# Performance work log

Hardware: AMD Instinct MI355X
Metric: run time of the kernel (lower is better)

The kernel has to match this reference:

```python
import jax, jax.numpy as jnp
import numpy as np

HEADS = 12
WINDOW = 128

def setup_inputs() -> dict:
    key = jax.random.key(0)
    ks = jax.random.split(key, 5)
    B, N, C = 1, 4096, 768
    return {
        'x': jax.random.normal(ks[0], (B, N, C), dtype=jnp.float32),
        'qkv_w': jax.random.normal(ks[1], (3 * C, C), dtype=jnp.float32) * 0.02,
        'qkv_b': jax.random.normal(ks[2], (3 * C,), dtype=jnp.float32) * 0.02,
        'proj_w': jax.random.normal(ks[3], (C, C), dtype=jnp.float32) * 0.02,
        'proj_b': jax.random.normal(ks[4], (C,), dtype=jnp.float32) * 0.02,
    }

def reference(x, qkv_w, qkv_b, proj_w, proj_b):
    B, N, C = x.shape
    H = HEADS
    hd = C // H
    # qkv projection (torch Linear: y = x @ W^T + b)
    qkv = x @ qkv_w.T + qkv_b                      # [B, N, 3C]
    qkv = qkv.reshape(B, N, 3, H, hd).transpose(2, 0, 3, 1, 4)  # [3, B, H, N, hd]
    q, k, v = qkv[0], qkv[1], qkv[2]               # each [B, H, N, hd]
    # local (banded) mask: |i - j| <= window_size
    idxs = jnp.arange(N)
    local = jnp.abs(idxs[:, None] - idxs[None, :]) <= WINDOW  # [N, N] bool
    # dense scores then mask (faithful to original O(N^2) math)
    attn = jnp.einsum('bhnd,bhmd->bhnm', q, k) / jnp.sqrt(jnp.float32(hd))
    attn = jnp.where(local[None, None], attn, -jnp.inf)
    attn = jax.nn.softmax(attn, axis=-1)
    out = jnp.einsum('bhnm,bhmd->bhnd', attn, v)   # [B, H, N, hd]
    out = out.transpose(0, 2, 1, 3).reshape(B, N, C)
    return out @ proj_w.T + proj_b
```

## Files before the change

### kernel.cpp

```cpp
#include <hip/hip_runtime.h>
#include <hip/hip_fp16.h>
#include <cmath>

typedef _Float16 f16;
typedef __attribute__((ext_vector_type(8))) _Float16 f16x8;
typedef __attribute__((ext_vector_type(4))) _Float16 f16x4;
typedef __attribute__((ext_vector_type(4))) float f32x4;

#define EXP2F(x) __builtin_amdgcn_exp2f(x)

__global__ void pack3_f32_f16(
    const float* __restrict__ s0, f16* __restrict__ d0, int nc0, int kc0,
    const float* __restrict__ s1, f16* __restrict__ d1, int nc1, int kc1,
    const float* __restrict__ s2, f16* __restrict__ d2, int nc2, int kc2)
{
    int wid  = (blockIdx.x * blockDim.x + threadIdx.x) >> 6;
    int lane = threadIdx.x & 63;
    const float* s; f16* d; int cid, KC;
    if (wid < nc0)                  { s = s0; d = d0; cid = wid;             KC = kc0; }
    else if (wid < nc0 + nc1)       { s = s1; d = d1; cid = wid - nc0;       KC = kc1; }
    else if (wid < nc0 + nc1 + nc2) { s = s2; d = d2; cid = wid - nc0 - nc1; KC = kc2; }
    else return;
    int rc = cid / KC, kc = cid % KC;
    int K  = KC << 5;
    const float* src = s + (size_t)(rc * 16 + (lane & 15)) * K + kc * 32 + (lane >> 4) * 8;
    float4 v0 = *(const float4*)src;
    float4 v1 = *(const float4*)(src + 4);
    f16x8 o = { (f16)v0.x, (f16)v0.y, (f16)v0.z, (f16)v0.w,
                (f16)v1.x, (f16)v1.y, (f16)v1.z, (f16)v1.w };
    *(f16x8*)(d + (size_t)cid * 512 + lane * 8) = o;
}

__device__ __forceinline__ void store4(f16* p, const f32x4& v) {
    f16x4 o = { (f16)v[0], (f16)v[1], (f16)v[2], (f16)v[3] };
    *(f16x4*)p = o;
}
__device__ __forceinline__ void store4(float* p, const f32x4& v) {
    float4 o = { v[0], v[1], v[2], v[3] };
    *(float4*)p = o;
}

template <int WR, int WC, int MT, int NT, int MODE, typename OT>
__global__ __launch_bounds__(256) void gemm_f16_packed(
    const f16* __restrict__ Ap,
    const f16* __restrict__ Wp,
    const float* __restrict__ bias,
    OT* __restrict__ out,
    int M, int N, int K)
{
    constexpr int KK  = 2;
    constexpr int ACH = WR * MT * KK;
    constexpr int BCH = WC * NT * KK;
    constexpr int AR  = ACH / 4;
    constexpr int BR  = BCH / 4;
    __shared__ f16 Ash[2][ACH * 512];
    __shared__ f16 Bsh[2][BCH * 512];

    const int tid  = threadIdx.x;
    const int lane = tid & 63;
    const int w    = tid >> 6;
    const int wr   = w / WC;
    const int wc   = w % WC;
    const int lr   = lane & 15;
    const int lq   = lane >> 4;
    const int bm   = blockIdx.y * (WR * MT * 16);
    const int bn   = blockIdx.x * (WC * NT * 16);
    const int KC   = K >> 5;

    const f16* ga[AR];
    const f16* gb[BR];
#pragma unroll
    for (int r = 0; r < AR; ++r) {
        int s = w * AR + r, rl = s / KK, kk = s % KK;
        ga[r] = Ap + ((size_t)((bm >> 4) + rl) * KC + kk) * 512 + lane * 8;
    }
#pragma unroll
    for (int r = 0; r < BR; ++r) {
        int s = w * BR + r, rl = s / KK, kk = s % KK;
        gb[r] = Wp + ((size_t)((bn >> 4) + rl) * KC + kk) * 512 + lane * 8;
    }

    f32x4 acc[MT][NT] = {};
    f16x8 sa[AR], sb[BR];

#pragma unroll
    for (int r = 0; r < AR; ++r) sa[r] = *(const f16x8*)(ga[r]);
#pragma unroll
    for (int r = 0; r < BR; ++r) sb[r] = *(const f16x8*)(gb[r]);
#pragma unroll
    for (int r = 0; r < AR; ++r) *(f16x8*)&Ash[0][(w * AR + r) * 512 + lane * 8] = sa[r];
#pragma unroll
    for (int r = 0; r < BR; ++r) *(f16x8*)&Bsh[0][(w * BR + r) * 512 + lane * 8] = sb[r];
    __syncthreads();

    const int nk = K >> 6;
    for (int k = 0; k < nk; ++k) {
        const int cur = k & 1;
        if (k + 1 < nk) {
            const int ko = (k + 1) * KK * 512;
#pragma unroll
            for (int r = 0; r < AR; ++r) sa[r] = *(const f16x8*)(ga[r] + ko);
#pragma unroll
            for (int r = 0; r < BR; ++r) sb[r] = *(const f16x8*)(gb[r] + ko);
        }
        f16x8 af[MT][KK], bf[NT][KK];
#pragma unroll
        for (int mt = 0; mt < MT; ++mt)
#pragma unroll
            for (int kk = 0; kk < KK; ++kk)
                af[mt][kk] = *(const f16x8*)&Ash[cur][((wr * MT + mt) * KK + kk) * 512 + lane * 8];
#pragma unroll
        for (int nt = 0; nt < NT; ++nt)
#pragma unroll
            for (int kk = 0; kk < KK; ++kk)
                bf[nt][kk] = *(const f16x8*)&Bsh[cur][((wc * NT + nt) * KK + kk) * 512 + lane * 8];
#pragma unroll
        for (int kk = 0; kk < KK; ++kk)
#pragma unroll
            for (int mt = 0; mt < MT; ++mt)
#pragma unroll
                for (int nt = 0; nt < NT; ++nt)
                    acc[mt][nt] = __builtin_amdgcn_mfma_f32_16x16x32_f16(
                        bf[nt][kk], af[mt][kk], acc[mt][nt], 0, 0, 0);
        if (k + 1 < nk) {
#pragma unroll
            for (int r = 0; r < AR; ++r)
                *(f16x8*)&Ash[cur ^ 1][(w * AR + r) * 512 + lane * 8] = sa[r];
#pragma unroll
            for (int r = 0; r < BR; ++r)
                *(f16x8*)&Bsh[cur ^ 1][(w * BR + r) * 512 + lane * 8] = sb[r];
        }
        __syncthreads();
    }

#pragma unroll
    for (int mt = 0; mt < MT; ++mt) {
        int row = bm + (wr * MT + mt) * 16 + lr;
#pragma unroll
        for (int nt = 0; nt < NT; ++nt) {
            int col = bn + (wc * NT + nt) * 16 + lq * 4;
            float4 bv = *(const float4*)(bias + col);
            f32x4 ov = acc[mt][nt];
            ov[0] += bv.x; ov[1] += bv.y; ov[2] += bv.z; ov[3] += bv.w;
            if (MODE == 0) {
                store4(out + (size_t)row * N + col, ov);
            } else {
                int tau = (col >= 1536) ? 2 : (col >= 768 ? 1 : 0);
                int rm  = col - tau * 768;
                int hh  = rm >> 6;
                int d   = rm & 63;
                f16* base = (f16*)out + ((size_t)tau * 12 + hh) * ((size_t)M * 64);
                if (tau < 2) {
                    size_t off = (size_t)(row >> 4) * 1024 + (d >> 5) * 512
                               + (size_t)((row & 15) + ((d >> 3) & 3) * 16) * 8 + (d & 7);
                    store4(base + off, ov);
                } else {
#pragma unroll
                    for (int i = 0; i < 4; ++i) {
                        int dd = d + i;
                        size_t off = (size_t)(dd >> 4) * ((size_t)M * 16)
                                   + (size_t)(row >> 5) * 512
                                   + (size_t)((dd & 15) + ((row >> 3) & 3) * 16) * 8 + (row & 7);
                        base[off] = (f16)ov[i];
                    }
                }
            }
        }
    }
}

#define WINDOW_SZ 128

__global__ __launch_bounds__(256) void local_attn_mfma(
    const f16* __restrict__ qkvp,
    f16* __restrict__ outp,
    int N)
{
    const int C = 768;
    __shared__ f16 Ps[4096];

    const int tid  = threadIdx.x;
    const int lane = tid & 63;
    const int w    = tid >> 6;
    const int r15  = lane & 15;
    const int q4   = lane >> 4;
    const int ntiles = N >> 6;
    const int h  = blockIdx.x / ntiles;
    const int i0 = (blockIdx.x % ntiles) << 6;

    const size_t hstride = (size_t)N * 64;
    const f16* Qh = qkvp + (size_t)h * hstride;
    const f16* Kh = qkvp + (size_t)(12 + h) * hstride;
    const f16* Vh = qkvp + (size_t)(24 + h) * hstride;
    const int dcStride = N * 16;

    f16x8 qf[2];
    {
        const f16* qp = Qh + (size_t)((i0 >> 4) + w) * 1024 + lane * 8;
        qf[0] = *(const f16x8*)(qp);
        qf[1] = *(const f16x8*)(qp + 512);
        const f16 qs = (f16)0.18033688f;
#pragma unroll
        for (int j = 0; j < 8; ++j) { qf[0][j] *= qs; qf[1][j] *= qs; }
    }

    f32x4 o[4] = {};
    float m_l = -1.0e30f, l_l = 0.f;

    const int lo = (i0 >= 128) ? 0 : ((128 - i0) >> 6);
    int hi = (N + 64 - i0) >> 6; if (hi > 4) hi = 4;

    const int lssr = lane ^ ((lane >> 3) & 7);

    for (int ch = lo; ch <= hi; ++ch) {
        const int jbase = i0 - 128 + ch * 64;
        const bool need_mask = (ch == 0) || (ch == 4);

        f32x4 s[4] = {};
#pragma unroll
        for (int ks = 0; ks < 2; ++ks)
#pragma unroll
            for (int nt = 0; nt < 4; ++nt) {
                f16x8 kf = *(const f16x8*)(Kh + (size_t)((jbase >> 4) + nt) * 1024
                                              + ks * 512 + lane * 8);
                s[nt] = __builtin_amdgcn_mfma_f32_16x16x32_f16(kf, qf[ks], s[nt], 0, 0, 0);
            }

        if (need_mask) {
            int qg = i0 + w * 16 + r15;
#pragma unroll
            for (int nt = 0; nt < 4; ++nt)
#pragma unroll
                for (int r = 0; r < 4; ++r) {
                    int dist = qg - (jbase + nt * 16 + q4 * 4 + r);
                    if (dist < 0) dist = -dist;
                    if (dist > WINDOW_SZ) s[nt][r] = -3.0e38f;
                }
        }

        float rmax = -3.0e38f;
#pragma unroll
        for (int nt = 0; nt < 4; ++nt)
#pragma unroll
            for (int r = 0; r < 4; ++r) rmax = fmaxf(rmax, s[nt][r]);
        rmax = fmaxf(rmax, __shfl_xor(rmax, 16));
        rmax = fmaxf(rmax, __shfl_xor(rmax, 32));
        float mn = fmaxf(m_l, rmax);
        float al = EXP2F(m_l - mn);
        m_l = mn;
        float rs = 0.f;
#pragma unroll
        for (int nt = 0; nt < 4; ++nt)
#pragma unroll
            for (int r = 0; r < 4; ++r) {
                float pv = EXP2F(s[nt][r] - mn);
                s[nt][r] = pv;
                rs += pv;
            }
        rs += __shfl_xor(rs, 16);
        rs += __shfl_xor(rs, 32);
        l_l = l_l * al + rs;
#pragma unroll
        for (int nd = 0; nd < 4; ++nd)
#pragma unroll
            for (int r = 0; r < 4; ++r) o[nd][r] *= al;

#pragma unroll
        for (int nt = 0; nt < 4; ++nt)
#pragma unroll
            for (int r = 0; r < 4; ++r) {
                int c  = nt * 16 + q4 * 4 + r;
                int cs = c >> 5;
                int c5 = c & 31;
                int ls = (c5 >> 3) * 16 + r15;
                int lss = ls ^ ((ls >> 3) & 7);
                Ps[(w * 2 + cs) * 512 + lss * 8 + (c5 & 7)] = (f16)s[nt][r];
            }

#pragma unroll
        for (int cs = 0; cs < 2; ++cs) {
            f16x8 pf = *(const f16x8*)&Ps[(w * 2 + cs) * 512 + lssr * 8];
#pragma unroll
            for (int nd = 0; nd < 4; ++nd) {
                f16x8 vf = *(const f16x8*)(Vh + (size_t)nd * dcStride
                                              + (size_t)((jbase >> 5) + cs) * 512 + lane * 8);
                o[nd] = __builtin_amdgcn_mfma_f32_16x16x32_f16(vf, pf, o[nd], 0, 0, 0);
            }
        }
    }

    float inv = 1.0f / l_l;
    const int KC2 = C >> 5;
    const int rc  = (i0 >> 4) + w;
#pragma unroll
    for (int nd = 0; nd < 4; ++nd) {
        int col = h * 64 + nd * 16 + q4 * 4;
        int kc  = col >> 5;
        int lp  = r15 + ((col >> 3) & 3) * 16;
        f16x4 ov = { (f16)(o[nd][0] * inv), (f16)(o[nd][1] * inv),
                     (f16)(o[nd][2] * inv), (f16)(o[nd][3] * inv) };
        *(f16x4*)(outp + ((size_t)rc * KC2 + kc) * 512 + lp * 8 + (col & 7)) = ov;
    }
}

extern "C" void kernel_launch(void* const* d_in, const int* in_sizes, int n_in,
                              void* d_out, int out_size, void* d_ws, size_t ws_size,
                              hipStream_t stream) {
    (void)n_in; (void)out_size; (void)ws_size;
    const float* x      = (const float*)d_in[0];
    const float* qkv_w  = (const float*)d_in[1];
    const float* qkv_b  = (const float*)d_in[2];
    const float* proj_w = (const float*)d_in[3];
    const float* proj_b = (const float*)d_in[4];
    float* outp = (float*)d_out;

    const int C    = in_sizes[2] / 3;
    const int Nseq = in_sizes[0] / C;
    const int C3   = 3 * C;
    const int KC   = C >> 5;

    char* ws = (char*)d_ws;
    f16* qkv_p = (f16*)ws;   ws += (size_t)Nseq * C3 * 2;
    f16* xp    = (f16*)ws;   ws += (size_t)Nseq * C * 2;
    f16* wqp   = (f16*)ws;   ws += (size_t)C3 * C * 2;
    f16* wpp   = (f16*)ws;
    f16* attn_p = xp;

    dim3 blk(256);
    {
        int nc0 = (Nseq / 16) * KC;
        int nc1 = (C3 / 16) * KC;
        int nc2 = (C / 16) * KC;
        int nwaves = nc0 + nc1 + nc2;
        pack3_f32_f16<<<dim3((nwaves + 3) / 4), blk, 0, stream>>>(
            x, xp, nc0, KC, qkv_w, wqp, nc1, KC, proj_w, wpp, nc2, KC);
    }
    gemm_f16_packed<2, 2, 4, 4, 1, f16><<<dim3(C3 / 128, Nseq / 128), blk, 0, stream>>>(
        xp, wqp, qkv_b, qkv_p, Nseq, C3, C);
    local_attn_mfma<<<dim3((C / 64) * (Nseq / 64)), blk, 0, stream>>>(
        qkv_p, attn_p, Nseq);
    gemm_f16_packed<2, 2, 2, 2, 0, float><<<dim3(C / 64, Nseq / 64), blk, 0, stream>>>(
        attn_p, wpp, proj_b, outp, Nseq, C, C);
}
```

Measured before the change: 130.6 us.

## Load QKV GEMM operands directly from global into registers, vectorize P stores

Adds a GEMM variant for the QKV projection that reads pre-packed MFMA fragments straight from global memory into registers, double-buffering them in registers instead of staging through shared memory with block barriers. The attention kernel's scatter of softmax probabilities into shared memory now writes four f16 values at once instead of scalar stores. This removes LDS traffic and __syncthreads from the QKV GEMM, but gives up cross-wave operand sharing, so each wave re-reads tiles from global/L2.

```diff
diff --git a/kernel.cpp b/kernel.cpp
--- a/kernel.cpp
+++ b/kernel.cpp
@@ -40,12 +40,115 @@
     *(float4*)p = o;
 }
 
-template <int WR, int WC, int MT, int NT, int MODE, typename OT>
-__global__ __launch_bounds__(256) void gemm_f16_packed(
+__device__ __forceinline__ void store_qkv(f16* out, int M, int row, int col,
+                                          const f32x4& ov) {
+    int tau = (col >= 1536) ? 2 : (col >= 768 ? 1 : 0);
+    int rm  = col - tau * 768;
+    int hh  = rm >> 6;
+    int d   = rm & 63;
+    f16* base = out + ((size_t)tau * 12 + hh) * ((size_t)M * 64);
+    if (tau < 2) {
+        size_t off = (size_t)(row >> 4) * 1024 + (d >> 5) * 512
+                   + (size_t)((row & 15) + ((d >> 3) & 3) * 16) * 8 + (d & 7);
+        store4(base + off, ov);
+    } else {
+#pragma unroll
+        for (int i = 0; i < 4; ++i) {
+            int dd = d + i;
+            size_t off = (size_t)(dd >> 4) * ((size_t)M * 16)
+                       + (size_t)(row >> 5) * 512
+                       + (size_t)((dd & 15) + ((row >> 3) & 3) * 16) * 8 + (row & 7);
+            base[off] = (f16)ov[i];
+        }
+    }
+}
+
+template <int MT, int NT, int MODE, typename OT>
+__global__ __launch_bounds__(256) void gemm_f16_direct(
     const f16* __restrict__ Ap,
     const f16* __restrict__ Wp,
     const float* __restrict__ bias,
     OT* __restrict__ out,
+    int M, int N, int K)
+{
+    const int tid  = threadIdx.x;
+    const int lane = tid & 63;
+    const int w    = tid >> 6;
+    const int wr   = w >> 1;
+    const int wc   = w & 1;
+    const int lr   = lane & 15;
+    const int lq   = lane >> 4;
+    const int bm   = blockIdx.y * (2 * MT * 16);
+    const int bn   = blockIdx.x * (2 * NT * 16);
+    const int KC   = K >> 5;
+
+    const f16* ga[MT];
+    const f16* gb[NT];
+#pragma unroll
+    for (int mt = 0; mt < MT; ++mt)
+        ga[mt] = Ap + (size_t)((bm >> 4) + wr * MT + mt) * KC * 512 + lane * 8;
+#pragma unroll
+    for (int nt = 0; nt < NT; ++nt)
+        gb[nt] = Wp + (size_t)((bn >> 4) + wc * NT + nt) * KC * 512 + lane * 8;
+
+    f32x4 acc[MT][NT] = {};
+    f16x8 a0[MT], b0[NT], a1[MT], b1[NT];
+
+#pragma unroll
+    for (int mt = 0; mt < MT; ++mt) a0[mt] = *(const f16x8*)(ga[mt]);
+#pragma unroll
+    for (int nt = 0; nt < NT; ++nt) b0[nt] = *(const f16x8*)(gb[nt]);
+
+    for (int k = 0; k < KC; k += 2) {
+        if (k + 1 < KC) {
+            const int off = (k + 1) * 512;
+#pragma unroll
+            for (int mt = 0; mt < MT; ++mt) a1[mt] = *(const f16x8*)(ga[mt] + off);
+#pragma unroll
+            for (int nt = 0; nt < NT; ++nt) b1[nt] = *(const f16x8*)(gb[nt] + off);
+        }
+#pragma unroll
+        for (int mt = 0; mt < MT; ++mt)
+#pragma unroll
+            for (int nt = 0; nt < NT; ++nt)
+                acc[mt][nt] = __builtin_amdgcn_mfma_f32_16x16x32_f16(
+                    b0[nt], a0[mt], acc[mt][nt], 0, 0, 0);
+        if (k + 2 < KC) {
+            const int off = (k + 2) * 512;
+#pragma unroll
+            for (int mt = 0; mt < MT; ++mt) a0[mt] = *(const f16x8*)(ga[mt] + off);
+#pragma unroll
+            for (int nt = 0; nt < NT; ++nt) b0[nt] = *(const f16x8*)(gb[nt] + off);
+        }
+        if (k + 1 < KC) {
+#pragma unroll
+            for (int mt = 0; mt < MT; ++mt)
+#pragma unroll
+                for (int nt = 0; nt < NT; ++nt)
+                    acc[mt][nt] = __builtin_amdgcn_mfma_f32_16x16x32_f16(
+                        b1[nt], a1[mt], acc[mt][nt], 0, 0, 0);
+        }
+    }
+
+#pragma unroll
+    for (int mt = 0; mt < MT; ++mt) {
+        int row = bm + (wr * MT + mt) * 16 + lr;
+#pragma unroll
+        for (int nt = 0; nt < NT; ++nt) {
+            int col = bn + (wc * NT + nt) * 16 + lq * 4;
+            float4 bv = *(const float4*)(bias + col);
+            f32x4 ov = acc[mt][nt];
+            ov[0] += bv.x; ov[1] += bv.y; ov[2] += bv.z; ov[3] += bv.w;
+            if (MODE == 0) store4((OT*)out + (size_t)row * N + col, ov);
+            else           store_qkv((f16*)out, M, row, col, ov);
+        }
+    }
+}
+
+template <int WR, int WC, int MT, int NT, typename OT>
+__global__ __launch_bounds__(256) void gemm_f16_packed(
+    const f16* __restrict__ Ap, const f16* __restrict__ Wp,
+    const float* __restrict__ bias, OT* __restrict__ out,
     int M, int N, int K)
 {
     constexpr int KK  = 2;
@@ -142,29 +245,7 @@
             float4 bv = *(const float4*)(bias + col);
             f32x4 ov = acc[mt][nt];
             ov[0] += bv.x; ov[1] += bv.y; ov[2] += bv.z; ov[3] += bv.w;
-            if (MODE == 0) {
-                store4(out + (size_t)row * N + col, ov);
-            } else {
-                int tau = (col >= 1536) ? 2 : (col >= 768 ? 1 : 0);
-                int rm  = col - tau * 768;
-                int hh  = rm >> 6;
-                int d   = rm & 63;
-                f16* base = (f16*)out + ((size_t)tau * 12 + hh) * ((size_t)M * 64);
-                if (tau < 2) {
-                    size_t off = (size_t)(row >> 4) * 1024 + (d >> 5) * 512
-                               + (size_t)((row & 15) + ((d >> 3) & 3) * 16) * 8 + (d & 7);
-                    store4(base + off, ov);
-                } else {
-#pragma unroll
-                    for (int i = 0; i < 4; ++i) {
-                        int dd = d + i;
-                        size_t off = (size_t)(dd >> 4) * ((size_t)M * 16)
-                                   + (size_t)(row >> 5) * 512
-                                   + (size_t)((dd & 15) + ((row >> 3) & 3) * 16) * 8 + (row & 7);
-                        base[off] = (f16)ov[i];
-                    }
-                }
-            }
+            store4(out + (size_t)row * N + col, ov);
         }
     }
 }
@@ -266,16 +347,13 @@
             for (int r = 0; r < 4; ++r) o[nd][r] *= al;
 
 #pragma unroll
-        for (int nt = 0; nt < 4; ++nt)
-#pragma unroll
-            for (int r = 0; r < 4; ++r) {
-                int c  = nt * 16 + q4 * 4 + r;
-                int cs = c >> 5;
-                int c5 = c & 31;
-                int ls = (c5 >> 3) * 16 + r15;
-                int lss = ls ^ ((ls >> 3) & 7);
-                Ps[(w * 2 + cs) * 512 + lss * 8 + (c5 & 7)] = (f16)s[nt][r];
-            }
+        for (int nt = 0; nt < 4; ++nt) {
+            int cs = nt >> 1;
+            int ls = ((nt & 1) * 2 + (q4 >> 1)) * 16 + r15;
+            int lss = ls ^ ((ls >> 3) & 7);
+            f16x4 pv4 = { (f16)s[nt][0], (f16)s[nt][1], (f16)s[nt][2], (f16)s[nt][3] };
+            *(f16x4*)&Ps[(w * 2 + cs) * 512 + lss * 8 + (q4 & 1) * 4] = pv4;
+        }
 
 #pragma unroll
         for (int cs = 0; cs < 2; ++cs) {
@@ -335,10 +413,10 @@
         pack3_f32_f16<<<dim3((nwaves + 3) / 4), blk, 0, stream>>>(
             x, xp, nc0, KC, qkv_w, wqp, nc1, KC, proj_w, wpp, nc2, KC);
     }
-    gemm_f16_packed<2, 2, 4, 4, 1, f16><<<dim3(C3 / 128, Nseq / 128), blk, 0, stream>>>(
-        xp, wqp, qkv_b, qkv_p, Nseq, C3, C);
+    gemm_f16_direct<4, 4, 1, f16><<<dim3(C3 / 128, Nseq / 128), blk, 0, stream>>>(
+        xp, wqp, qkv_b, (f16*)qkv_p, Nseq, C3, C);
     local_attn_mfma<<<dim3((C / 64) * (Nseq / 64)), blk, 0, stream>>>(
         qkv_p, attn_p, Nseq);
-    gemm_f16_packed<2, 2, 2, 2, 0, float><<<dim3(C / 64, Nseq / 64), blk, 0, stream>>>(
+    gemm_f16_packed<2, 2, 2, 2, float><<<dim3(C / 64, Nseq / 64), blk, 0, stream>>>(
         attn_p, wpp, proj_b, outp, Nseq, C, C);
 }
```

Measured after the change: 131.1 us. No clear change (+0.4%).
